# Kernel optimization log

Hardware: AMD Instinct MI355X
Metric: run time of the kernel (lower is better)

The kernel has to match this reference:

```python
import jax, jax.numpy as jnp
import numpy as np

B, C, H, W = 32, 1024, 48, 24
P = 3            # num_parts
IC = C // 8      # inter_channels for position attention
PH = H // P      # part height


def setup_inputs() -> dict:
    key = jax.random.key(0)
    ks = jax.random.split(key, 16)
    s = 0.02
    return {
        "x": jax.random.normal(ks[0], (B, C, H, W), jnp.float32),
        "modality": jax.random.randint(ks[1], (B,), 0, 2),
        # per-part 1x1 conv weights (stacked over parts)
        "Wq": jax.random.normal(ks[2], (P, IC, C), jnp.float32) * s,
        "bq": jnp.zeros((P, IC), jnp.float32),
        "Wk": jax.random.normal(ks[3], (P, IC, C), jnp.float32) * s,
        "bk": jnp.zeros((P, IC), jnp.float32),
        "Wv": jax.random.normal(ks[4], (P, C, C), jnp.float32) * s,
        "bv": jnp.zeros((P, C), jnp.float32),
        # gamma residual scales (torch inits to 0; random so output differs from x)
        "gamma_pa": jax.random.normal(ks[5], (P,), jnp.float32) * 0.1,
        "gamma_ca": jax.random.normal(ks[6], (P,), jnp.float32) * 0.1,
        # modality gate: Linear(1,64) -> ReLU -> Linear(64,P) -> Sigmoid
        "gW1": jax.random.normal(ks[7], (64, 1), jnp.float32) * 0.01,
        "gb1": jnp.zeros((64,), jnp.float32),
        "gW2": jax.random.normal(ks[8], (P, 64), jnp.float32) * 0.01,
        "gb2": jnp.zeros((P,), jnp.float32),
    }


def _part_dual_attn(part, Wq, bq, Wk, bk, Wv, bv, g_pa, g_ca):
    # part: [B, C, ph, W]
    b, c, ph, w = part.shape
    n = ph * w
    xf = part.reshape(b, c, n)  # [B,C,N]
    # --- Position attention (PAM) ---
    q = jnp.einsum('oc,bcn->bno', Wq, xf) + bq            # [B,N,IC]
    k = jnp.einsum('oc,bcn->bon', Wk, xf) + bk[:, None]   # [B,IC,N]
    attn = jax.nn.softmax(jnp.einsum('bno,bom->bnm', q, k), axis=-1)  # [B,N,N]
    v = jnp.einsum('oc,bcn->bon', Wv, xf) + bv[:, None]   # [B,C,N]
    pa = jnp.einsum('bcn,bmn->bcm', v, attn).reshape(part.shape)
    pa = g_pa * pa + part
    # --- Channel attention (CAM) with max-shifted softmax ---
    e = jnp.einsum('bcn,bdn->bcd', xf, xf)                # [B,C,C]
    e = jnp.max(e, axis=-1, keepdims=True) - e
    ca_attn = jax.nn.softmax(e, axis=-1)
    ca = jnp.einsum('bcd,bdn->bcn', ca_attn, xf).reshape(part.shape)
    ca = g_ca * ca + part
    return pa + ca


def reference(x, modality, Wq, bq, Wk, bk, Wv, bv, gamma_pa, gamma_ca, gW1, gb1, gW2, gb2):
    b = x.shape[0]
    # modality gate -> per-sample per-part blend weights [B,P]
    m = modality.astype(jnp.float32)[:, None]
    h = jax.nn.relu(m @ gW1.T + gb1)
    w_gate = jax.nn.sigmoid(h @ gW2.T + gb2)              # [B,P]
    # split into P horizontal parts: [P,B,C,ph,W]
    parts = x.reshape(b, C, P, PH, W).transpose(2, 0, 1, 3, 4)
    part_outs = jax.vmap(_part_dual_attn)(parts, Wq, bq, Wk, bk, Wv, bv, gamma_pa, gamma_ca)
    wp = w_gate.T[:, :, None, None, None]                 # [P,B,1,1,1]
    blended = parts * (1.0 - wp) + part_outs * wp         # [P,B,C,ph,W]
    return blended.transpose(1, 2, 0, 3, 4).reshape(b, C, H, W)
```

## Files before the change

kernel.cpp:

```cpp
#include <hip/hip_runtime.h>
#include <hip/hip_bf16.h>
#include <cstdint>

constexpr int kB  = 32;
constexpr int kC  = 1024;
constexpr int kH  = 48;
constexpr int kW  = 24;
constexpr int kP  = 3;
constexpr int kPH = 16;
constexpr int kN  = kPH * kW;
constexpr int kHW = kH * kW;
constexpr int64_t kCHW = (int64_t)kC * kHW;

typedef __attribute__((ext_vector_type(8))) short short8b;
typedef __attribute__((ext_vector_type(4))) float f32x4;

__device__ __forceinline__ void gl_lds16(const void* g, void* l) {
    __builtin_amdgcn_global_load_lds(
        (const __attribute__((address_space(1))) void*)g,
        (__attribute__((address_space(3))) void*)l, 16, 0, 0);
}

__device__ __forceinline__ void swz_block(int& bx, int& by, int& bz) {
    const int gx = gridDim.x, gy = gridDim.y, gz = gridDim.z;
    if ((gz & 7) == 0) {
        const int tpp = gx * gy;
        const int L   = (blockIdx.z * gy + blockIdx.y) * gx + blockIdx.x;
        const int xcd = L & 7;
        const int idx = L >> 3;
        const int ppx = gz >> 3;
        const int pairL = idx / tpp;
        const int tile  = idx - pairL * tpp;
        bz = xcd * ppx + pairL;
        by = tile / gx;
        bx = tile - by * gx;
    } else {
        bx = blockIdx.x; by = blockIdx.y; bz = blockIdx.z;
    }
}

#define WAIT8()       asm volatile("s_waitcnt vmcnt(8)" ::: "memory")
#define WAIT0()       asm volatile("s_waitcnt vmcnt(0)" ::: "memory")
#define RAW_BARRIER() asm volatile("s_barrier" ::: "memory")
#define SFENCE()      __builtin_amdgcn_sched_barrier(0)

__global__ void gate_kernel(const int* __restrict__ modality,
                            const float* __restrict__ gW1, const float* __restrict__ gb1,
                            const float* __restrict__ gW2, const float* __restrict__ gb2,
                            const float* __restrict__ gpa, const float* __restrict__ gca,
                            const float* __restrict__ bq, const float* __restrict__ bk,
                            float* __restrict__ wg, float* __restrict__ cpa,
                            float* __restrict__ cca, float* __restrict__ bqk)
{
    const int t = threadIdx.x;
    if (t < 768) {
        const int p = t >> 8, o = t & 255;
        bqk[t] = (o < 128) ? bq[p * 128 + o] : bk[p * 128 + (o - 128)];
    }
    if (t < kB * kP) {
        const int b = t / kP, p = t % kP;
        const float m = (float)modality[b];
        float acc = gb2[p];
        #pragma unroll
        for (int j = 0; j < 64; ++j) {
            float h = fmaxf(fmaf(m, gW1[j], gb1[j]), 0.0f);
            acc = fmaf(gW2[p * 64 + j], h, acc);
        }
        const float w = 1.0f / (1.0f + __expf(-acc));
        wg[t]  = w;
        cpa[t] = w * gpa[p];
        cca[t] = w * gca[p];
    }
}

__global__ __launch_bounds__(256)
void wcast_kernel(const float* __restrict__ Wq, const float* __restrict__ Wk,
                  const float* __restrict__ Wv,
                  __hip_bfloat16* __restrict__ Wqkb, __hip_bfloat16* __restrict__ Wvb)
{
    const int64_t i = (int64_t)blockIdx.x * 256 + threadIdx.x;
    if (i < 196608) {
        const int64_t e = i * 4;
        const int p = (int)(e / 262144);
        const int rem = (int)(e % 262144);
        const int o = rem / 1024, c = rem % 1024;
        const float* s = (o < 128) ? (Wq + (int64_t)p * 131072 + (int64_t)o * 1024 + c)
                                   : (Wk + (int64_t)p * 131072 + (int64_t)(o - 128) * 1024 + c);
        float4 v = *(const float4*)s;
        __hip_bfloat16* d = Wqkb + e;
        d[0] = __float2bfloat16(v.x); d[1] = __float2bfloat16(v.y);
        d[2] = __float2bfloat16(v.z); d[3] = __float2bfloat16(v.w);
    } else if (i < 196608 + 786432) {
        const int64_t e = (i - 196608) * 4;
        float4 v = *(const float4*)(Wv + e);
        __hip_bfloat16* d = Wvb + e;
        d[0] = __float2bfloat16(v.x); d[1] = __float2bfloat16(v.y);
        d[2] = __float2bfloat16(v.z); d[3] = __float2bfloat16(v.w);
    }
}

__global__ void zeroz_kernel(float* __restrict__ Z)
{
    Z[(int64_t)blockIdx.x * 1024 + threadIdx.x] = 0.0f;
}

__global__ __launch_bounds__(256)
void cast_tr_kernel(const float* __restrict__ x,
                    __hip_bfloat16* __restrict__ xfb,
                    __hip_bfloat16* __restrict__ xfT)
{
    int bx, by, bz;
    swz_block(bx, by, bz);
    const int j = bz;
    const int bb = j / kP, pp = j % kP;
    const float* src = x + (int64_t)bb * kCHW + pp * kN;
    const int c0 = bx * 32, n0 = by * 32;
    __shared__ float tile[32][33];
    const int tx = threadIdx.x & 31, ty = threadIdx.x >> 5;
    #pragma unroll
    for (int r = 0; r < 4; ++r) {
        const int cl = ty * 4 + r;
        const int c = c0 + cl;
        float v = src[(int64_t)c * kHW + n0 + tx];
        xfb[(int64_t)j * 393216 + (int64_t)c * kN + n0 + tx] = __float2bfloat16(v);
        tile[tx][cl] = v;
    }
    __syncthreads();
    #pragma unroll
    for (int r = 0; r < 4; ++r) {
        const int nl = ty * 4 + r;
        xfT[(int64_t)j * 393216 + (int64_t)(n0 + nl) * kC + c0 + tx] =
            __float2bfloat16(tile[nl][tx]);
    }
}

template<int BIAS>
__global__ __launch_bounds__(256, 2)
void mm_kernel(const __hip_bfloat16* __restrict__ A0, int64_t aSB, int64_t aSP, int lda,
               const __hip_bfloat16* __restrict__ B0, int64_t bSB, int64_t bSP, int ldb,
               __hip_bfloat16* __restrict__ C0, int64_t cSB, int64_t cSP, int ldc,
               const float* __restrict__ bias0, int biasSP, int K)
{
    __shared__ char lds[65536];

    int bx, by, bz;
    swz_block(bx, by, bz);
    const int j = bz, bb = j / kP, pp = j % kP;
    const char* Ab = (const char*)(A0 + (int64_t)bb * aSB + (int64_t)pp * aSP);
    const char* Bb = (const char*)(B0 + (int64_t)bb * bSB + (int64_t)pp * bSP);
    const int m0 = bx * 128, n0 = by * 128;
    const int t = threadIdx.x, lane = t & 63, wv = t >> 6;
    const int wm = (wv & 1) * 64, wn = (wv >> 1) * 64;
    const size_t ldab = (size_t)lda * 2, ldbb = (size_t)ldb * 2;

    const int rr   = wv * 8 + (lane >> 3);
    const int gsrc = ((lane & 7) ^ (lane >> 3)) * 16;
    const int lrow = (wv * 8 + (lane >> 3)) * 128 + (lane & 7) * 16;

    auto STAGE = [&](int buf, int k0) {
        const char* Asrc = Ab + (size_t)(m0 + rr) * ldab + (size_t)k0 * 2 + gsrc;
        const char* Bsrc = Bb + (size_t)(n0 + rr) * ldbb + (size_t)k0 * 2 + gsrc;
        char* As = lds + buf * 32768;
        char* Bs = As + 16384;
        #pragma unroll
        for (int i = 0; i < 4; ++i) {
            gl_lds16(Asrc + (size_t)i * 32 * ldab, As + i * 4096 + lrow);
            gl_lds16(Bsrc + (size_t)i * 32 * ldbb, Bs + i * 4096 + lrow);
        }
    };

    f32x4 acc[4][4];
    #pragma unroll
    for (int a = 0; a < 4; ++a)
        #pragma unroll
        for (int b = 0; b < 4; ++b) acc[a][b] = (f32x4){0.f, 0.f, 0.f, 0.f};

    const int nk = K >> 6;
    STAGE(0, 0);
    int cur = 0;
    for (int k = 0; k < nk; ++k) {
        if (k + 1 < nk) { STAGE(cur ^ 1, (k + 1) << 6); WAIT8(); }
        else            { WAIT0(); }
        SFENCE();
        RAW_BARRIER();
        const char* As = lds + cur * 32768;
        const char* Bs = As + 16384;
        #pragma unroll
        for (int kk = 0; kk < 2; ++kk) {
            const int gpos = ((kk * 4 + (lane >> 4)) ^ (lane & 7)) * 16;
            short8b af[4], bf[4];
            #pragma unroll
            for (int f = 0; f < 4; ++f) {
                af[f] = *(const short8b*)(As + (wm + f * 16 + (lane & 15)) * 128 + gpos);
                bf[f] = *(const short8b*)(Bs + (wn + f * 16 + (lane & 15)) * 128 + gpos);
            }
            #pragma unroll
            for (int fm = 0; fm < 4; ++fm)
                #pragma unroll
                for (int fn = 0; fn < 4; ++fn)
                    acc[fm][fn] = __builtin_amdgcn_mfma_f32_16x16x32_bf16(
                        af[fm], bf[fn], acc[fm][fn], 0, 0, 0);
        }
        RAW_BARRIER();
        cur ^= 1;
    }

    __hip_bfloat16* Cm = C0 + (int64_t)bb * cSB + (int64_t)pp * cSP;
    #pragma unroll
    for (int fn = 0; fn < 4; ++fn) {
        const int col = n0 + wn + fn * 16 + (lane & 15);
        const float cb = (BIAS == 2) ? bias0[pp * biasSP + col] : 0.0f;
        #pragma unroll
        for (int fm = 0; fm < 4; ++fm)
            #pragma unroll
            for (int jr = 0; jr < 4; ++jr) {
                const int row = m0 + wm + fm * 16 + (lane >> 4) * 4 + jr;
                Cm[(int64_t)row * ldc + col] = __float2bfloat16(acc[fm][fn][jr] + cb);
            }
    }
}

__global__ __launch_bounds__(256, 2)
void ecam_kernel(const __hip_bfloat16* __restrict__ xfb,
                 __hip_bfloat16* __restrict__ eb,
                 float* __restrict__ Z)
{
    __shared__ char lds[65536];

    int bx, by, bz;
    swz_block(bx, by, bz);
    const int j = bz;
    int bi = 0;
    while ((bi + 1) * (bi + 2) / 2 <= bx) ++bi;
    const int bj = bx - bi * (bi + 1) / 2;
    const char* Ab = (const char*)(xfb + (int64_t)j * 393216);
    const int m0 = bi * 128, n0 = bj * 128;
    const int t = threadIdx.x, lane = t & 63, wv = t >> 6;
    const int wm = (wv & 1) * 64, wn = (wv >> 1) * 64;
    constexpr size_t ldab = 768;

    const int rr   = wv * 8 + (lane >> 3);
    const int gsrc = ((lane & 7) ^ (lane >> 3)) * 16;
    const int lrow = (wv * 8 + (lane >> 3)) * 128 + (lane & 7) * 16;

    auto STAGE = [&](int buf, int k0) {
        const char* Asrc = Ab + (size_t)(m0 + rr) * ldab + (size_t)k0 * 2 + gsrc;
        const char* Bsrc = Ab + (size_t)(n0 + rr) * ldab + (size_t)k0 * 2 + gsrc;
        char* As = lds + buf * 32768;
        char* Bs = As + 16384;
        #pragma unroll
        for (int i = 0; i < 4; ++i) {
            gl_lds16(Asrc + (size_t)i * 32 * ldab, As + i * 4096 + lrow);
            gl_lds16(Bsrc + (size_t)i * 32 * ldab, Bs + i * 4096 + lrow);
        }
    };

    f32x4 acc[4][4];
    #pragma unroll
    for (int a = 0; a < 4; ++a)
        #pragma unroll
        for (int b = 0; b < 4; ++b) acc[a][b] = (f32x4){0.f, 0.f, 0.f, 0.f};

    STAGE(0, 0);
    int cur = 0;
    for (int k = 0; k < 6; ++k) {
        if (k + 1 < 6) { STAGE(cur ^ 1, (k + 1) << 6); WAIT8(); }
        else           { WAIT0(); }
        SFENCE();
        RAW_BARRIER();
        const char* As = lds + cur * 32768;
        const char* Bs = As + 16384;
        #pragma unroll
        for (int kk = 0; kk < 2; ++kk) {
            const int gpos = ((kk * 4 + (lane >> 4)) ^ (lane & 7)) * 16;
            short8b af[4], bf[4];
            #pragma unroll
            for (int f = 0; f < 4; ++f) {
                af[f] = *(const short8b*)(As + (wm + f * 16 + (lane & 15)) * 128 + gpos);
                bf[f] = *(const short8b*)(Bs + (wn + f * 16 + (lane & 15)) * 128 + gpos);
            }
            #pragma unroll
            for (int fm = 0; fm < 4; ++fm)
                #pragma unroll
                for (int fn = 0; fn < 4; ++fn)
                    acc[fm][fn] = __builtin_amdgcn_mfma_f32_16x16x32_bf16(
                        af[fm], bf[fn], acc[fm][fn], 0, 0, 0);
        }
        RAW_BARRIER();
        cur ^= 1;
    }

    #pragma unroll
    for (int fm = 0; fm < 4; ++fm)
        #pragma unroll
        for (int fn = 0; fn < 4; ++fn)
            #pragma unroll
            for (int jr = 0; jr < 4; ++jr)
                acc[fm][fn][jr] = __expf(-60.f - acc[fm][fn][jr]);

    __hip_bfloat16* Cm = eb + (int64_t)j * 1048576;
    float* Zp = Z + (int64_t)j * 1024;

    #pragma unroll
    for (int fm = 0; fm < 4; ++fm)
        #pragma unroll
        for (int jr = 0; jr < 4; ++jr) {
            const int row = m0 + wm + fm * 16 + (lane >> 4) * 4 + jr;
            float v = 0.f;
            #pragma unroll
            for (int fn = 0; fn < 4; ++fn) {
                const int col = n0 + wn + fn * 16 + (lane & 15);
                Cm[(int64_t)row * 1024 + col] = __float2bfloat16(acc[fm][fn][jr]);
                v += acc[fm][fn][jr];
            }
            v += __shfl_xor(v, 1);
            v += __shfl_xor(v, 2);
            v += __shfl_xor(v, 4);
            v += __shfl_xor(v, 8);
            if ((lane & 15) == 0) atomicAdd(Zp + row, v);
        }

    if (bi != bj) {
        #pragma unroll
        for (int fn = 0; fn < 4; ++fn) {
            const int col = n0 + wn + fn * 16 + (lane & 15);
            float v2 = 0.f;
            #pragma unroll
            for (int fm = 0; fm < 4; ++fm) {
                const int row0 = m0 + wm + fm * 16 + (lane >> 4) * 4;
                __hip_bfloat16 h0 = __float2bfloat16(acc[fm][fn][0]);
                __hip_bfloat16 h1 = __float2bfloat16(acc[fm][fn][1]);
                __hip_bfloat16 h2 = __float2bfloat16(acc[fm][fn][2]);
                __hip_bfloat16 h3 = __float2bfloat16(acc[fm][fn][3]);
                ushort4 w4;
                w4.x = *(ushort*)&h0; w4.y = *(ushort*)&h1;
                w4.z = *(ushort*)&h2; w4.w = *(ushort*)&h3;
                *(ushort4*)((ushort*)Cm + (int64_t)col * 1024 + row0) = w4;
                v2 += (acc[fm][fn][0] + acc[fm][fn][1]) +
                      (acc[fm][fn][2] + acc[fm][fn][3]);
            }
            v2 += __shfl_xor(v2, 16);
            v2 += __shfl_xor(v2, 32);
            if ((lane >> 4) == 0) atomicAdd(Zp + col, v2);
        }
    }
}

__global__ __launch_bounds__(256, 2)
void ep_cam_kernel(const __hip_bfloat16* __restrict__ Wvb,
                   const __hip_bfloat16* __restrict__ yTb,
                   const __hip_bfloat16* __restrict__ eb,
                   const __hip_bfloat16* __restrict__ xfT,
                   const float* __restrict__ Z,
                   const float* __restrict__ x,
                   float* __restrict__ out,
                   const float* __restrict__ wg,
                   const float* __restrict__ cpa,
                   const float* __restrict__ cca,
                   const float* __restrict__ bv)
{
    __shared__ char lds[65536];

    int bx, by, bz;
    swz_block(bx, by, bz);
    const int j = bz, bb = j / kP, pp = j % kP;
    const int m0 = bx * 128, n0 = by * 128;
    const int t = threadIdx.x, lane = t & 63, wv = t >> 6;
    const int wm = (wv & 1) * 64, wn = (wv >> 1) * 64;

    const int rr   = wv * 8 + (lane >> 3);
    const int gsrc = ((lane & 7) ^ (lane >> 3)) * 16;
    const int lrow = (wv * 8 + (lane >> 3)) * 128 + (lane & 7) * 16;

    const char* AbW = (const char*)(Wvb + (int64_t)pp * 1048576);
    const char* AbE = (const char*)(eb  + (int64_t)j  * 1048576);
    const char* BbY = (const char*)(yTb + (int64_t)j * 393216);
    const char* BbX = (const char*)(xfT + (int64_t)j * 393216);

    auto STAGE = [&](int buf, int g) {
        const char* A = (g < 16) ? AbW : AbE;
        const char* B = (g < 16) ? BbY : BbX;
        const size_t k0b = (size_t)(g & 15) * 128;
        const char* Asrc = A + (size_t)(m0 + rr) * 2048 + k0b + gsrc;
        const char* Bsrc = B + (size_t)(n0 + rr) * 2048 + k0b + gsrc;
        char* As = lds + buf * 32768;
        char* Bs = As + 16384;
        #pragma unroll
        for (int i = 0; i < 4; ++i) {
            gl_lds16(Asrc + (size_t)i * 32 * 2048, As + i * 4096 + lrow);
            gl_lds16(Bsrc + (size_t)i * 32 * 2048, Bs + i * 4096 + lrow);
        }
    };

    f32x4 accA[4][4], accB[4][4];
    #pragma unroll
    for (int a = 0; a < 4; ++a)
        #pragma unroll
        for (int b = 0; b < 4; ++b) {
            accA[a][b] = (f32x4){0.f, 0.f, 0.f, 0.f};
            accB[a][b] = (f32x4){0.f, 0.f, 0.f, 0.f};
        }

    auto DOMFMA = [&](f32x4 (&acc)[4][4], const char* As, const char* Bs) {
        #pragma unroll
        for (int kk = 0; kk < 2; ++kk) {
            const int gpos = ((kk * 4 + (lane >> 4)) ^ (lane & 7)) * 16;
            short8b af[4], bf[4];
            #pragma unroll
            for (int f = 0; f < 4; ++f) {
                af[f] = *(const short8b*)(As + (wm + f * 16 + (lane & 15)) * 128 + gpos);
                bf[f] = *(const short8b*)(Bs + (wn + f * 16 + (lane & 15)) * 128 + gpos);
            }
            #pragma unroll
            for (int fm = 0; fm < 4; ++fm)
                #pragma unroll
                for (int fn = 0; fn < 4; ++fn)
                    acc[fm][fn] = __builtin_amdgcn_mfma_f32_16x16x32_bf16(
                        af[fm], bf[fn], acc[fm][fn], 0, 0, 0);
        }
    };

    STAGE(0, 0);
    int cur = 0;
    #pragma unroll
    for (int half = 0; half < 2; ++half) {
        for (int kt = 0; kt < 16; ++kt) {
            const int g = half * 16 + kt;
            if (g + 1 < 32) { STAGE(cur ^ 1, g + 1); WAIT8(); }
            else            { WAIT0(); }
            SFENCE();
            RAW_BARRIER();
            const char* As = lds + cur * 32768;
            const char* Bs = As + 16384;
            if (half == 0) DOMFMA(accA, As, Bs);
            else           DOMFMA(accB, As, Bs);
            RAW_BARRIER();
            cur ^= 1;
        }
    }

    const float gsc = 1.0f + wg[j];
    const float cfp = cpa[j];
    const float cfc = cca[j];
    const float* Xm = x   + (int64_t)bb * kCHW + pp * kN;
    float*       Om = out + (int64_t)bb * kCHW + pp * kN;
    const float* Zp = Z + (int64_t)j * 1024;
    #pragma unroll
    for (int fm = 0; fm < 4; ++fm)
        #pragma unroll
        for (int jr = 0; jr < 4; ++jr) {
            const int row = m0 + wm + fm * 16 + (lane >> 4) * 4 + jr;
            const float rb = cfp * bv[pp * 1024 + row];
            const float zs = cfc / Zp[row];
            #pragma unroll
            for (int fn = 0; fn < 4; ++fn) {
                const int col = n0 + wn + fn * 16 + (lane & 15);
                const int64_t off = (int64_t)row * kHW + col;
                Om[off] = fmaf(gsc, Xm[off],
                               accA[fm][fn][jr] + rb + zs * accB[fm][fn][jr]);
            }
        }
}

__global__ __launch_bounds__(64) void sm_pam(__hip_bfloat16* __restrict__ buf,
                                             const float* __restrict__ scale,
                                             int chPairs)
{
    const int L = blockIdx.x;
    int pair, row;
    if ((chPairs & 7) == 0) {
        const int xcd = L & 7, idx = L >> 3;
        pair = xcd * (chPairs >> 3) + idx / kN;
        row  = idx % kN;
    } else { pair = L / kN; row = L % kN; }
    __hip_bfloat16* rp = buf + (int64_t)pair * (kN * kN) + (int64_t)row * kN;
    const int t = threadIdx.x;
    float v[6];
    float mx = -3.402823466e38f;
    #pragma unroll
    for (int r = 0; r < 6; ++r) {
        v[r] = __bfloat162float(rp[t + 64 * r]);
        mx = fmaxf(mx, v[r]);
    }
    #pragma unroll
    for (int off = 32; off > 0; off >>= 1) mx = fmaxf(mx, __shfl_xor(mx, off));
    float s = 0.0f;
    #pragma unroll
    for (int r = 0; r < 6; ++r) { v[r] = __expf(v[r] - mx); s += v[r]; }
    #pragma unroll
    for (int off = 32; off > 0; off >>= 1) s += __shfl_xor(s, off);
    const float inv = scale[pair] / s;
    #pragma unroll
    for (int r = 0; r < 6; ++r) rp[t + 64 * r] = __float2bfloat16(v[r] * inv);
}

extern "C" void kernel_launch(void* const* d_in, const int* in_sizes, int n_in,
                              void* d_out, int out_size, void* d_ws, size_t ws_size,
                              hipStream_t stream)
{
    const float* x   = (const float*)d_in[0];
    const int*   mod = (const int*)d_in[1];
    const float* Wq  = (const float*)d_in[2];
    const float* bq  = (const float*)d_in[3];
    const float* Wk  = (const float*)d_in[4];
    const float* bk  = (const float*)d_in[5];
    const float* Wv  = (const float*)d_in[6];
    const float* bv  = (const float*)d_in[7];
    const float* gpa = (const float*)d_in[8];
    const float* gca = (const float*)d_in[9];
    const float* gW1 = (const float*)d_in[10];
    const float* gb1 = (const float*)d_in[11];
    const float* gW2 = (const float*)d_in[12];
    const float* gb2 = (const float*)d_in[13];
    float* out = (float*)d_out;

    const int chList[5] = {48, 24, 12, 6, 3};
    int CH = 3;
    for (int i = 0; i < 5; ++i) {
        size_t need = 7868544ull + (size_t)chList[i] * 4952064ull;
        if (need <= ws_size) { CH = chList[i]; break; }
    }
    const int NCHUNK = 96 / CH;

    char* ws = (char*)d_ws;
    __hip_bfloat16* Wqkb = (__hip_bfloat16*)(ws + 0);
    __hip_bfloat16* Wvb  = (__hip_bfloat16*)(ws + 1572864);
    float* bqk = (float*)(ws + 7864320);
    float* wg  = (float*)(ws + 7867392);
    float* cpa = (float*)(ws + 7867776);
    float* cca = (float*)(ws + 7868160);
    __hip_bfloat16* xfT   = (__hip_bfloat16*)(ws + 7868544);
    __hip_bfloat16* xfb   = xfT   + (int64_t)CH * 393216;
    __hip_bfloat16* qkT   = xfb   + (int64_t)CH * 393216;
    __hip_bfloat16* attnb = qkT   + (int64_t)CH * 98304;
    __hip_bfloat16* yTb   = attnb + (int64_t)CH * 147456;
    __hip_bfloat16* eb    = yTb   + (int64_t)CH * 393216;
    float*          Zbuf  = (float*)(eb + (int64_t)CH * 1048576);

    gate_kernel<<<1, 768, 0, stream>>>(mod, gW1, gb1, gW2, gb2, gpa, gca, bq, bk,
                                       wg, cpa, cca, bqk);
    wcast_kernel<<<3840, 256, 0, stream>>>(Wq, Wk, Wv, Wqkb, Wvb);

    for (int ch = 0; ch < NCHUNK; ++ch) {
        const int pair0 = ch * CH;
        const int b0 = pair0 / kP;
        const float* xc   = x   + (int64_t)b0 * kCHW;
        float*       outc = out + (int64_t)b0 * kCHW;

        cast_tr_kernel<<<dim3(32, 12, CH), 256, 0, stream>>>(xc, xfb, xfT);
        zeroz_kernel<<<CH, 1024, 0, stream>>>(Zbuf);

        mm_kernel<2><<<dim3(3, 2, CH), 256, 0, stream>>>(
            xfT, 3 * 393216, 393216, 1024,
            Wqkb, 0, 262144, 1024,
            qkT, 3 * 98304, 98304, 256,
            bqk, 256, 1024);
        mm_kernel<0><<<dim3(3, 3, CH), 256, 0, stream>>>(
            qkT, 3 * 98304, 98304, 256,
            qkT + 128, 3 * 98304, 98304, 256,
            attnb, 3 * 147456, 147456, 384,
            nullptr, 0, 128);
        sm_pam<<<CH * kN, 64, 0, stream>>>(attnb, cpa + pair0, CH);
        mm_kernel<0><<<dim3(3, 8, CH), 256, 0, stream>>>(
            attnb, 3 * 147456, 147456, 384,
            xfb, 3 * 393216, 393216, 384,
            yTb, 3 * 393216, 393216, 1024,
            nullptr, 0, 384);
        ecam_kernel<<<dim3(36, 1, CH), 256, 0, stream>>>(xfb, eb, Zbuf);
        ep_cam_kernel<<<dim3(8, 3, CH), 256, 0, stream>>>(
            Wvb, yTb, eb, xfT, Zbuf, xc, outc,
            wg + pair0, cpa + pair0, cca + pair0, bv);
    }
}
```

Baseline: 537.3 us.

## Merge CAM and PAM accumulators, triple-buffer smaller K tiles, raise occupancy

```diff
diff --git a/kernel.cpp b/kernel.cpp
--- a/kernel.cpp
+++ b/kernel.cpp
@@ -40,6 +40,7 @@
 }
 
 #define WAIT8()       asm volatile("s_waitcnt vmcnt(8)" ::: "memory")
+#define WAIT4()       asm volatile("s_waitcnt vmcnt(4)" ::: "memory")
 #define WAIT0()       asm volatile("s_waitcnt vmcnt(0)" ::: "memory")
 #define RAW_BARRIER() asm volatile("s_barrier" ::: "memory")
 #define SFENCE()      __builtin_amdgcn_sched_barrier(0)
@@ -346,7 +347,7 @@
     }
 }
 
-__global__ __launch_bounds__(256, 2)
+__global__ __launch_bounds__(256, 3)
 void ep_cam_kernel(const __hip_bfloat16* __restrict__ Wvb,
                    const __hip_bfloat16* __restrict__ yTb,
                    const __hip_bfloat16* __restrict__ eb,
@@ -359,7 +360,7 @@
                    const float* __restrict__ cca,
                    const float* __restrict__ bv)
 {
-    __shared__ char lds[65536];
+    __shared__ char lds[49152];
 
     int bx, by, bz;
     swz_block(bx, by, bz);
@@ -368,9 +369,9 @@
     const int t = threadIdx.x, lane = t & 63, wv = t >> 6;
     const int wm = (wv & 1) * 64, wn = (wv >> 1) * 64;
 
-    const int rr   = wv * 8 + (lane >> 3);
-    const int gsrc = ((lane & 7) ^ (lane >> 3)) * 16;
-    const int lrow = (wv * 8 + (lane >> 3)) * 128 + (lane & 7) * 16;
+    const int rr4  = lane >> 2;
+    const int gsrc = (((lane & 3) ^ (rr4 & 3)) * 16);
+    const int ldst = lane * 16;
 
     const char* AbW = (const char*)(Wvb + (int64_t)pp * 1048576);
     const char* AbE = (const char*)(eb  + (int64_t)j  * 1048576);
@@ -378,86 +379,94 @@
     const char* BbX = (const char*)(xfT + (int64_t)j * 393216);
 
     auto STAGE = [&](int buf, int g) {
-        const char* A = (g < 16) ? AbW : AbE;
-        const char* B = (g < 16) ? BbY : BbX;
-        const size_t k0b = (size_t)(g & 15) * 128;
-        const char* Asrc = A + (size_t)(m0 + rr) * 2048 + k0b + gsrc;
-        const char* Bsrc = B + (size_t)(n0 + rr) * 2048 + k0b + gsrc;
-        char* As = lds + buf * 32768;
-        char* Bs = As + 16384;
-        #pragma unroll
-        for (int i = 0; i < 4; ++i) {
-            gl_lds16(Asrc + (size_t)i * 32 * 2048, As + i * 4096 + lrow);
-            gl_lds16(Bsrc + (size_t)i * 32 * 2048, Bs + i * 4096 + lrow);
+        const char* A = (g < 32) ? AbE : AbW;
+        const char* B = (g < 32) ? BbX : BbY;
+        const size_t k0b = (size_t)(g & 31) * 64;
+        const char* Asrc = A + (size_t)(m0 + wv * 32 + rr4) * 2048 + k0b + gsrc;
+        const char* Bsrc = B + (size_t)(n0 + wv * 32 + rr4) * 2048 + k0b + gsrc;
+        char* As = lds + buf * 16384;
+        char* Bs = As + 8192;
+        #pragma unroll
+        for (int i = 0; i < 2; ++i) {
+            gl_lds16(Asrc + (size_t)i * 16 * 2048, As + wv * 2048 + i * 1024 + ldst);
+            gl_lds16(Bsrc + (size_t)i * 16 * 2048, Bs + wv * 2048 + i * 1024 + ldst);
         }
     };
 
-    f32x4 accA[4][4], accB[4][4];
+    const float cfc = cca[j];
+    const float* Zp = Z + (int64_t)j * 1024;
+    float zsc[4][4];
+    #pragma unroll
+    for (int fm = 0; fm < 4; ++fm)
+        #pragma unroll
+        for (int jr = 0; jr < 4; ++jr) {
+            const int row = m0 + wm + fm * 16 + (lane >> 4) * 4 + jr;
+            zsc[fm][jr] = cfc / Zp[row];
+        }
+
+    f32x4 acc[4][4];
     #pragma unroll
     for (int a = 0; a < 4; ++a)
         #pragma unroll
-        for (int b = 0; b < 4; ++b) {
-            accA[a][b] = (f32x4){0.f, 0.f, 0.f, 0.f};
-            accB[a][b] = (f32x4){0.f, 0.f, 0.f, 0.f};
-        }
-
-    auto DOMFMA = [&](f32x4 (&acc)[4][4], const char* As, const char* Bs) {
-        #pragma unroll
-        for (int kk = 0; kk < 2; ++kk) {
-            const int gpos = ((kk * 4 + (lane >> 4)) ^ (lane & 7)) * 16;
-            short8b af[4], bf[4];
-            #pragma unroll
-            for (int f = 0; f < 4; ++f) {
-                af[f] = *(const short8b*)(As + (wm + f * 16 + (lane & 15)) * 128 + gpos);
-                bf[f] = *(const short8b*)(Bs + (wn + f * 16 + (lane & 15)) * 128 + gpos);
-            }
+        for (int b = 0; b < 4; ++b) acc[a][b] = (f32x4){0.f, 0.f, 0.f, 0.f};
+
+    const int gpos = ((lane >> 4) ^ (lane & 3)) * 16;
+
+    STAGE(0, 0);
+    STAGE(1, 1);
+    int cur = 0;
+    for (int g = 0; g < 64; ++g) {
+        if (g < 62) {
+            int nb = cur + 2; if (nb >= 3) nb -= 3;
+            STAGE(nb, g + 2);
+            WAIT8();
+        } else if (g == 62) { WAIT4(); }
+        else                { WAIT0(); }
+        SFENCE();
+        RAW_BARRIER();
+        if (g == 32) {
             #pragma unroll
             for (int fm = 0; fm < 4; ++fm)
                 #pragma unroll
-                for (int fn = 0; fn < 4; ++fn)
-                    acc[fm][fn] = __builtin_amdgcn_mfma_f32_16x16x32_bf16(
-                        af[fm], bf[fn], acc[fm][fn], 0, 0, 0);
-        }
-    };
-
-    STAGE(0, 0);
-    int cur = 0;
-    #pragma unroll
-    for (int half = 0; half < 2; ++half) {
-        for (int kt = 0; kt < 16; ++kt) {
-            const int g = half * 16 + kt;
-            if (g + 1 < 32) { STAGE(cur ^ 1, g + 1); WAIT8(); }
-            else            { WAIT0(); }
-            SFENCE();
-            RAW_BARRIER();
-            const char* As = lds + cur * 32768;
-            const char* Bs = As + 16384;
-            if (half == 0) DOMFMA(accA, As, Bs);
-            else           DOMFMA(accB, As, Bs);
-            RAW_BARRIER();
-            cur ^= 1;
-        }
+                for (int jr = 0; jr < 4; ++jr) {
+                    const float zs = zsc[fm][jr];
+                    #pragma unroll
+                    for (int fn = 0; fn < 4; ++fn) acc[fm][fn][jr] *= zs;
+                }
+        }
+        const char* As = lds + cur * 16384;
+        const char* Bs = As + 8192;
+        short8b af[4], bf[4];
+        #pragma unroll
+        for (int f = 0; f < 4; ++f) {
+            af[f] = *(const short8b*)(As + (wm + f * 16 + (lane & 15)) * 64 + gpos);
+            bf[f] = *(const short8b*)(Bs + (wn + f * 16 + (lane & 15)) * 64 + gpos);
+        }
+        #pragma unroll
+        for (int fm = 0; fm < 4; ++fm)
+            #pragma unroll
+            for (int fn = 0; fn < 4; ++fn)
+                acc[fm][fn] = __builtin_amdgcn_mfma_f32_16x16x32_bf16(
+                    af[fm], bf[fn], acc[fm][fn], 0, 0, 0);
+        RAW_BARRIER();
+        if (++cur == 3) cur = 0;
     }
 
     const float gsc = 1.0f + wg[j];
     const float cfp = cpa[j];
-    const float cfc = cca[j];
     const float* Xm = x   + (int64_t)bb * kCHW + pp * kN;
     float*       Om = out + (int64_t)bb * kCHW + pp * kN;
-    const float* Zp = Z + (int64_t)j * 1024;
     #pragma unroll
     for (int fm = 0; fm < 4; ++fm)
         #pragma unroll
         for (int jr = 0; jr < 4; ++jr) {
             const int row = m0 + wm + fm * 16 + (lane >> 4) * 4 + jr;
             const float rb = cfp * bv[pp * 1024 + row];
-            const float zs = cfc / Zp[row];
             #pragma unroll
             for (int fn = 0; fn < 4; ++fn) {
                 const int col = n0 + wn + fn * 16 + (lane & 15);
                 const int64_t off = (int64_t)row * kHW + col;
-                Om[off] = fmaf(gsc, Xm[off],
-                               accA[fm][fn][jr] + rb + zs * accB[fm][fn][jr]);
+                Om[off] = fmaf(gsc, Xm[off], acc[fm][fn][jr] + rb);
             }
         }
 }
@@ -514,9 +523,9 @@
     const float* gb2 = (const float*)d_in[13];
     float* out = (float*)d_out;
 
-    const int chList[5] = {48, 24, 12, 6, 3};
+    const int chList[6] = {96, 48, 24, 12, 6, 3};
     int CH = 3;
-    for (int i = 0; i < 5; ++i) {
+    for (int i = 0; i < 6; ++i) {
         size_t need = 7868544ull + (size_t)chList[i] * 4952064ull;
         if (need <= ws_size) { CH = chList[i]; break; }
     }
```

New measurement: 563.4 us. 1.05x slower.
